# Performance work log

Hardware: AMD Instinct MI355X
Metric: run time of the kernel (lower is better)

## Reference

```python
import jax, jax.numpy as jnp
import numpy as np

EPS = 1e-5

def layer_norm(x, gamma, beta):
    mu = jnp.mean(x, axis=-1, keepdims=True)
    var = jnp.mean(jnp.square(x - mu), axis=-1, keepdims=True)
    return (x - mu) * jax.lax.rsqrt(var + EPS) * gamma + beta

def setup_inputs() -> dict:
    key = jax.random.key(0)
    ks = jax.random.split(key, 16)
    B, Cq, Hq, Wq = 8, 256, 32, 32
    Cc, Hc, Wc = 512, 64, 64
    def lin(k, fan_in, fan_out):
        lim = 1.0 / np.sqrt(fan_in)
        k1, k2 = jax.random.split(k)
        W = jax.random.uniform(k1, (fan_in, fan_out), jnp.float32, -lim, lim)
        b = jax.random.uniform(k2, (fan_out,), jnp.float32, -lim, lim)
        return W, b
    Wq_, bq = lin(ks[0], Cq, Cq)
    Wk_, bk = lin(ks[1], Cc, Cq)
    Wv_, bv = lin(ks[2], Cc, Cq)
    Wo_, bo = lin(ks[3], Cq, Cq)
    return {
        "query": jax.random.normal(ks[4], (B, Cq, Hq, Wq), jnp.float32),
        "context": jax.random.normal(ks[5], (B, Cc, Hc, Wc), jnp.float32),
        "Wq": Wq_, "bq": bq, "Wk": Wk_, "bk": bk, "Wv": Wv_, "bv": bv,
        "Wo": Wo_, "bo": bo,
        "gq": jnp.ones((Cq,), jnp.float32), "betq": jnp.zeros((Cq,), jnp.float32),
        "gc": jnp.ones((Cc,), jnp.float32), "betc": jnp.zeros((Cc,), jnp.float32),
    }

def reference(query, context, Wq, bq, Wk, bk, Wv, bv, Wo, bo, gq, betq, gc, betc):
    B, Cq, Hq, Wq_sp = query.shape
    _, Cc, Hc, Wc = context.shape
    num_heads = 8
    head_dim = Cq // num_heads
    scale = jnp.sqrt(jnp.float32(head_dim))
    N = Hq * Wq_sp
    # adaptive_avg_pool2d with divisible sizes == average pooling over equal bins
    ctx = context.reshape(B, Cc, Hq, Hc // Hq, Wq_sp, Wc // Wq_sp).mean(axis=(3, 5))
    q_flat = query.reshape(B, Cq, N).transpose(0, 2, 1)          # (B,N,Cq)
    c_flat = ctx.reshape(B, Cc, N).transpose(0, 2, 1)            # (B,N,Cc)
    qn = layer_norm(q_flat, gq, betq)
    cn = layer_norm(c_flat, gc, betc)
    q = (qn @ Wq + bq).reshape(B, N, num_heads, head_dim).transpose(0, 2, 1, 3)
    k = (cn @ Wk + bk).reshape(B, N, num_heads, head_dim).transpose(0, 2, 1, 3)
    v = (cn @ Wv + bv).reshape(B, N, num_heads, head_dim).transpose(0, 2, 1, 3)
    attn = jnp.einsum('bhnd,bhmd->bhnm', q, k) / scale
    attn = jax.nn.softmax(attn, axis=-1)
    out = jnp.einsum('bhnm,bhmd->bhnd', attn, v)
    out = out.transpose(0, 2, 1, 3).reshape(B, N, Cq)
    out = out @ Wo + bo
    out = q_flat + out                                           # residual
    return out.transpose(0, 2, 1).reshape(B, Cq, Hq, Wq_sp)
```

## Files before the change

### kernel.cpp

```cpp
#include <hip/hip_runtime.h>
#include <hip/hip_bf16.h>
#include <cstddef>

#define B_  8
#define CQ  256
#define CC  512
#define N_  1024
#define HQ  32
#define WQ  32
#define NH  8
#define HD  32

typedef __bf16 bf16x8 __attribute__((ext_vector_type(8)));
typedef float f32x4 __attribute__((ext_vector_type(4)));
typedef float f32x16 __attribute__((ext_vector_type(16)));
typedef unsigned int uint4v __attribute__((ext_vector_type(4)));
typedef unsigned short ushort8 __attribute__((ext_vector_type(8)));
typedef unsigned short ushort4v __attribute__((ext_vector_type(4)));

__device__ __forceinline__ unsigned short f2bf(float x) {
    return __builtin_bit_cast(unsigned short, __float2bfloat16(x));
}
__device__ __forceinline__ float bf2f(unsigned short x) {
    return __bfloat162float(__builtin_bit_cast(__hip_bfloat16, x));
}
__device__ __forceinline__ bf16x8 ldb8(const unsigned short* p) {
    return __builtin_bit_cast(bf16x8, *(const ushort8*)p);
}

__global__ __launch_bounds__(256) void prep_k(
    const float* __restrict__ query, const float* __restrict__ context,
    const float* __restrict__ Wq, const float* __restrict__ Wk,
    const float* __restrict__ Wv, const float* __restrict__ Wo,
    const float* __restrict__ gq, const float* __restrict__ betq,
    const float* __restrict__ gc, const float* __restrict__ betc,
    __hip_bfloat16* __restrict__ Wqt, __hip_bfloat16* __restrict__ Wkt,
    __hip_bfloat16* __restrict__ Wvt, __hip_bfloat16* __restrict__ Wot,
    __hip_bfloat16* __restrict__ qn, __hip_bfloat16* __restrict__ cn) {
    __shared__ float T[32][33];
    __shared__ float SsA[32][16];
    __shared__ float S2A[32][16];
    __shared__ float SsB[16][64];
    __shared__ float S2B[16][64];
    __shared__ float Mu[64], Rs[64];

    const int bid = blockIdx.x;
    const int tid = threadIdx.x;

    if (bid < 512) {
        const int x = bid & 15, y = (bid >> 4) & 7, z = bid >> 7;
        const float* W; __hip_bfloat16* Wt; int K;
        switch (z) {
            case 0: W = Wq; Wt = Wqt; K = CQ; break;
            case 1: W = Wk; Wt = Wkt; K = CC; break;
            case 2: W = Wv; Wt = Wvt; K = CC; break;
            default: W = Wo; Wt = Wot; K = CQ; break;
        }
        const int k0 = x * 32;
        if (k0 >= K) return;
        const int c0 = y * 32;
        const int tx = tid & 31, ty = tid >> 5;
        #pragma unroll
        for (int i = 0; i < 4; ++i) {
            const int r = ty + 8 * i;
            T[r][tx] = W[(size_t)(k0 + r) * CQ + c0 + tx];
        }
        __syncthreads();
        #pragma unroll
        for (int i = 0; i < 4; ++i) {
            const int r = ty + 8 * i;
            Wt[(size_t)(c0 + r) * K + k0 + tx] = __float2bfloat16(T[tx][r]);
        }
    } else if (bid < 1024) {
        const int u    = bid - 512;
        const int wqc2 = u & 1, hq = (u >> 1) & 31, b = u >> 6;
        const int pp   = tid & 7;
        const int cg   = tid >> 3;
        const int ch0  = cg * 16;

        const float* Cb = context + ((size_t)b * CC + ch0) * 4096
                        + (size_t)(2 * hq) * 64 + (32 * wqc2 + 4 * pp);
        float pv0[16], pv1[16];
        float ss0 = 0.f, ss1 = 0.f, s20 = 0.f, s21 = 0.f;
        #pragma unroll
        for (int i = 0; i < 16; ++i) {
            const float4 r0 = *(const float4*)(Cb + (size_t)i * 4096);
            const float4 r1 = *(const float4*)(Cb + (size_t)i * 4096 + 64);
            const float v0 = (r0.x + r0.y + r1.x + r1.y) * 0.25f;
            const float v1 = (r0.z + r0.w + r1.z + r1.w) * 0.25f;
            pv0[i] = v0; pv1[i] = v1;
            ss0 += v0; s20 += v0 * v0;
            ss1 += v1; s21 += v1 * v1;
        }
        SsA[cg][2 * pp]     = ss0; S2A[cg][2 * pp]     = s20;
        SsA[cg][2 * pp + 1] = ss1; S2A[cg][2 * pp + 1] = s21;
        __syncthreads();
        if (tid < 16) {
            float ts = 0.f, t2 = 0.f;
            #pragma unroll
            for (int i = 0; i < 32; ++i) { ts += SsA[i][tid]; t2 += S2A[i][tid]; }
            const float mu  = ts * (1.f / CC);
            const float var = t2 * (1.f / CC) - mu * mu;
            Mu[tid] = mu; Rs[tid] = rsqrtf(var + 1e-5f);
        }
        __syncthreads();
        const float mu0 = Mu[2 * pp],     rs0 = Rs[2 * pp];
        const float mu1 = Mu[2 * pp + 1], rs1 = Rs[2 * pp + 1];
        const int pos0 = hq * 32 + wqc2 * 16 + 2 * pp;
        unsigned short* dst = (unsigned short*)cn
            + ((size_t)b * N_ + pos0) * CC + ch0;
        ushort8 a0, a1, b0, b1;
        #pragma unroll
        for (int i = 0; i < 8; ++i) {
            a0[i] = f2bf((pv0[i] - mu0) * rs0 * gc[ch0 + i] + betc[ch0 + i]);
            b0[i] = f2bf((pv1[i] - mu1) * rs1 * gc[ch0 + i] + betc[ch0 + i]);
        }
        #pragma unroll
        for (int i = 0; i < 8; ++i) {
            a1[i] = f2bf((pv0[8 + i] - mu0) * rs0 * gc[ch0 + 8 + i] + betc[ch0 + 8 + i]);
            b1[i] = f2bf((pv1[8 + i] - mu1) * rs1 * gc[ch0 + 8 + i] + betc[ch0 + 8 + i]);
        }
        *(ushort8*)(dst)          = a0;
        *(ushort8*)(dst + 8)      = a1;
        *(ushort8*)(dst + CC)     = b0;
        *(ushort8*)(dst + CC + 8) = b1;
    } else {
        const int u  = bid - 1024;
        const int nt = u & 15, b = u >> 4;
        const int nq = tid & 15;
        const int cg = tid >> 4;
        const int ch0 = cg * 16;
        const int nb  = nt * 64 + 4 * nq;

        const float* Qb = query + ((size_t)b * CQ + ch0) * N_ + nb;
        float qv[64];
        float ps[4] = {0.f, 0.f, 0.f, 0.f};
        float p2[4] = {0.f, 0.f, 0.f, 0.f};
        #pragma unroll
        for (int i = 0; i < 16; ++i) {
            const float4 v = *(const float4*)(Qb + (size_t)i * N_);
            qv[4 * i + 0] = v.x; qv[4 * i + 1] = v.y;
            qv[4 * i + 2] = v.z; qv[4 * i + 3] = v.w;
            ps[0] += v.x; p2[0] += v.x * v.x;
            ps[1] += v.y; p2[1] += v.y * v.y;
            ps[2] += v.z; p2[2] += v.z * v.z;
            ps[3] += v.w; p2[3] += v.w * v.w;
        }
        #pragma unroll
        for (int j = 0; j < 4; ++j) {
            SsB[cg][4 * nq + j] = ps[j];
            S2B[cg][4 * nq + j] = p2[j];
        }
        __syncthreads();
        if (tid < 64) {
            float ts = 0.f, t2 = 0.f;
            #pragma unroll
            for (int i = 0; i < 16; ++i) { ts += SsB[i][tid]; t2 += S2B[i][tid]; }
            const float mu  = ts * (1.f / CQ);
            const float var = t2 * (1.f / CQ) - mu * mu;
            Mu[tid] = mu; Rs[tid] = rsqrtf(var + 1e-5f);
        }
        __syncthreads();
        #pragma unroll
        for (int j = 0; j < 4; ++j) {
            const float mu = Mu[4 * nq + j], rs = Rs[4 * nq + j];
            ushort8 o0, o1;
            #pragma unroll
            for (int i = 0; i < 8; ++i)
                o0[i] = f2bf((qv[4 * i + j] - mu) * rs * gq[ch0 + i] + betq[ch0 + i]);
            #pragma unroll
            for (int i = 0; i < 8; ++i)
                o1[i] = f2bf((qv[4 * (8 + i) + j] - mu) * rs * gq[ch0 + 8 + i] + betq[ch0 + 8 + i]);
            unsigned short* dst = (unsigned short*)qn
                + ((size_t)b * N_ + nb + j) * CQ + ch0;
            *(ushort8*)(dst)     = o0;
            *(ushort8*)(dst + 8) = o1;
        }
    }
}

__global__ __launch_bounds__(256) void proj_all_k(
    const __hip_bfloat16* __restrict__ qn, const __hip_bfloat16* __restrict__ cn,
    const __hip_bfloat16* __restrict__ Wqt, const __hip_bfloat16* __restrict__ Wkt,
    const __hip_bfloat16* __restrict__ Wvt,
    const float* __restrict__ bq, const float* __restrict__ bk,
    const float* __restrict__ bv,
    __hip_bfloat16* __restrict__ Qb, __hip_bfloat16* __restrict__ Kb,
    __hip_bfloat16* __restrict__ Vt, float qsc) {
    __shared__ unsigned short As[64][40];
    __shared__ unsigned short B1[64][40];
    __shared__ unsigned short B2[64][40];

    const int zz = blockIdx.z;
    const int n0 = blockIdx.x * 64;
    const int c0 = blockIdx.y * 64;
    const int tid = threadIdx.x;
    const int wid = tid >> 6, lane = tid & 63;
    const int lg = lane >> 4, ln = lane & 15;
    const int wn0 = (wid & 1) * 32, wc0 = (wid >> 1) * 32;
    const int sr = tid >> 2;
    const int sk = (tid & 3) * 8;

    if (zz >= 8) {
        const int b = zz - 8;
        const unsigned short* Ab = (const unsigned short*)qn + ((size_t)b * N_ + n0) * CQ;
        const unsigned short* Wb = (const unsigned short*)Wqt + (size_t)c0 * CQ;
        f32x4 acc[2][2] = {};
        ushort8 ra = *(const ushort8*)(Ab + (size_t)sr * CQ + sk);
        ushort8 rw = *(const ushort8*)(Wb + (size_t)sr * CQ + sk);
        for (int t = 0; t < 8; ++t) {
            *(ushort8*)&As[sr][sk] = ra;
            *(ushort8*)&B1[sr][sk] = rw;
            __syncthreads();
            if (t < 7) {
                ra = *(const ushort8*)(Ab + (size_t)sr * CQ + (t + 1) * 32 + sk);
                rw = *(const ushort8*)(Wb + (size_t)sr * CQ + (t + 1) * 32 + sk);
            }
            bf16x8 a[2], w[2];
            #pragma unroll
            for (int i = 0; i < 2; ++i) a[i] = ldb8(&As[wn0 + 16 * i + ln][8 * lg]);
            #pragma unroll
            for (int j = 0; j < 2; ++j) w[j] = ldb8(&B1[wc0 + 16 * j + ln][8 * lg]);
            #pragma unroll
            for (int i = 0; i < 2; ++i)
                #pragma unroll
                for (int j = 0; j < 2; ++j)
                    acc[i][j] = __builtin_amdgcn_mfma_f32_16x16x32_bf16(a[i], w[j], acc[i][j], 0, 0, 0);
            __syncthreads();
        }
        #pragma unroll
        for (int j = 0; j < 2; ++j) {
            const int co = c0 + wc0 + 16 * j + ln;
            const int h = co >> 5, d = co & 31;
            const float bb = bq[co];
            #pragma unroll
            for (int i = 0; i < 2; ++i)
                #pragma unroll
                for (int r = 0; r < 4; ++r) {
                    const int n = n0 + wn0 + 16 * i + 4 * lg + r;
                    Qb[(((size_t)b * NH + h) * N_ + n) * HD + d] =
                        __float2bfloat16((acc[i][j][r] + bb) * qsc);
                }
        }
    } else {
        const int b = zz;
        const unsigned short* Ab  = (const unsigned short*)cn + ((size_t)b * N_ + n0) * CC;
        const unsigned short* Wkb = (const unsigned short*)Wkt + (size_t)c0 * CC;
        const unsigned short* Wvb = (const unsigned short*)Wvt + (size_t)c0 * CC;
        f32x4 accK[2][2] = {};
        f32x4 accV[2][2] = {};
        ushort8 ra = *(const ushort8*)(Ab  + (size_t)sr * CC + sk);
        ushort8 rk = *(const ushort8*)(Wkb + (size_t)sr * CC + sk);
        ushort8 rv = *(const ushort8*)(Wvb + (size_t)sr * CC + sk);
        for (int t = 0; t < 16; ++t) {
            *(ushort8*)&As[sr][sk] = ra;
            *(ushort8*)&B1[sr][sk] = rk;
            *(ushort8*)&B2[sr][sk] = rv;
            __syncthreads();
            if (t < 15) {
                ra = *(const ushort8*)(Ab  + (size_t)sr * CC + (t + 1) * 32 + sk);
                rk = *(const ushort8*)(Wkb + (size_t)sr * CC + (t + 1) * 32 + sk);
                rv = *(const ushort8*)(Wvb + (size_t)sr * CC + (t + 1) * 32 + sk);
            }
            bf16x8 a[2], wk[2], wv[2];
            #pragma unroll
            for (int i = 0; i < 2; ++i) {
                a[i]  = ldb8(&As[wn0 + 16 * i + ln][8 * lg]);
                wk[i] = ldb8(&B1[wc0 + 16 * i + ln][8 * lg]);
                wv[i] = ldb8(&B2[wc0 + 16 * i + ln][8 * lg]);
            }
            #pragma unroll
            for (int i = 0; i < 2; ++i)
                #pragma unroll
                for (int j = 0; j < 2; ++j) {
                    accK[i][j] = __builtin_amdgcn_mfma_f32_16x16x32_bf16(a[i], wk[j], accK[i][j], 0, 0, 0);
                    accV[i][j] = __builtin_amdgcn_mfma_f32_16x16x32_bf16(a[i], wv[j], accV[i][j], 0, 0, 0);
                }
            __syncthreads();
        }
        #pragma unroll
        for (int j = 0; j < 2; ++j) {
            const int co = c0 + wc0 + 16 * j + ln;
            const int h = co >> 5, d = co & 31;
            const float bbk = bk[co], bbv = bv[co];
            #pragma unroll
            for (int i = 0; i < 2; ++i) {
                const int nb = n0 + wn0 + 16 * i + 4 * lg;
                #pragma unroll
                for (int r = 0; r < 4; ++r)
                    Kb[(((size_t)b * NH + h) * N_ + nb + r) * HD + d] =
                        __float2bfloat16(accK[i][j][r] + bbk);
                ushort4v o;
                #pragma unroll
                for (int r = 0; r < 4; ++r) o[r] = f2bf(accV[i][j][r] + bbv);
                const int g  = (nb >> 2) & 3;
                const int gp = ((g & 1) << 1) | (g >> 1);
                const int nbp = (nb & ~15) | (gp << 2);
                *(ushort4v*)((unsigned short*)Vt + (((size_t)b * NH + h) * HD + d) * N_ + nbp) = o;
            }
        }
    }
}

__global__ __launch_bounds__(256) void attn32_k(
    const __hip_bfloat16* __restrict__ Q,
    const __hip_bfloat16* __restrict__ K,
    const __hip_bfloat16* __restrict__ Vt,
    __hip_bfloat16* __restrict__ O) {
    __shared__ float accS[2][64][20];
    __shared__ float lwS[2][64];

    const int lin = blockIdx.x + 16 * blockIdx.y;
    const int eff = (lin & 7) * 128 + (lin >> 3);
    const int qt  = eff & 15;
    const int bh  = eff >> 4;
    const int b   = bh >> 3;
    const int h   = bh & 7;
    const int wid  = threadIdx.x >> 6;
    const int lane = threadIdx.x & 63;
    const int l31  = lane & 31;
    const int hh   = lane >> 5;
    const int qsub = wid >> 1;
    const int kvh  = wid & 1;
    const int q0   = qt * 64 + qsub * 32;

    const unsigned short* Qp = (const unsigned short*)Q + ((size_t)bh * N_ + q0) * HD;
    const unsigned short* Kbb = (const unsigned short*)K + (size_t)bh * N_ * HD;
    const unsigned short* Vb = (const unsigned short*)Vt + ((size_t)bh * HD + l31) * N_;

    bf16x8 qB[2];
    #pragma unroll
    for (int m = 0; m < 2; ++m)
        qB[m] = ldb8(Qp + (size_t)l31 * HD + 16 * m + 8 * hh);

    const f32x16 Z = {0.f,0.f,0.f,0.f,0.f,0.f,0.f,0.f,
                      0.f,0.f,0.f,0.f,0.f,0.f,0.f,0.f};
    f32x16 acc = Z;
    float ls0 = 0.f, ls1 = 0.f, ls2 = 0.f, ls3 = 0.f;

    const int kvbase = kvh * 512;
    const unsigned short* kp = Kbb + (size_t)(kvbase + l31) * HD + 8 * hh;
    const unsigned short* vp = Vb + kvbase + 8 * hh;

    bf16x8 kaA[2][4];
    #pragma unroll
    for (int j = 0; j < 4; ++j)
        kaA[0][j] = ldb8(kp + (j >> 1) * 1024 + (j & 1) * 16);

    #pragma unroll
    for (int st = 0; st < 8; ++st) {
        const int cur = st & 1;
        bf16x8 va[4];
        #pragma unroll
        for (int j = 0; j < 4; ++j)
            va[j] = ldb8(vp + st * 64 + 16 * j);
        if (st < 7) {
            const unsigned short* kp2 = kp + (size_t)(st + 1) * 2048;
            #pragma unroll
            for (int j = 0; j < 4; ++j)
                kaA[cur ^ 1][j] = ldb8(kp2 + (j >> 1) * 1024 + (j & 1) * 16);
        }

        f32x16 s0, s1;
        s0 = __builtin_amdgcn_mfma_f32_32x32x16_bf16(kaA[cur][0], qB[0], Z, 0, 0, 0);
        s0 = __builtin_amdgcn_mfma_f32_32x32x16_bf16(kaA[cur][1], qB[1], s0, 0, 0, 0);
        s1 = __builtin_amdgcn_mfma_f32_32x32x16_bf16(kaA[cur][2], qB[0], Z, 0, 0, 0);
        s1 = __builtin_amdgcn_mfma_f32_32x32x16_bf16(kaA[cur][3], qB[1], s1, 0, 0, 0);

        unsigned int pk[2][4][2];
        #pragma unroll
        for (int T = 0; T < 2; ++T) {
            float p[16];
            #pragma unroll
            for (int r = 0; r < 16; ++r)
                p[r] = __builtin_amdgcn_exp2f(T == 0 ? s0[r] : s1[r]);
            #pragma unroll
            for (int r = 0; r < 16; r += 4) {
                ls0 += p[r]; ls1 += p[r + 1]; ls2 += p[r + 2]; ls3 += p[r + 3];
            }
            #pragma unroll
            for (int c = 0; c < 4; ++c) {
                asm("v_cvt_pk_bf16_f32 %0, %1, %2"
                    : "=v"(pk[T][c][0]) : "v"(p[4 * c]), "v"(p[4 * c + 1]));
                asm("v_cvt_pk_bf16_f32 %0, %1, %2"
                    : "=v"(pk[T][c][1]) : "v"(p[4 * c + 2]), "v"(p[4 * c + 3]));
            }
        }

        #pragma unroll
        for (int w = 0; w < 4; ++w) {
            const int T = w >> 1, cp = w & 1;
            uint4v fu = {pk[T][2 * cp][0], pk[T][2 * cp][1],
                         pk[T][2 * cp + 1][0], pk[T][2 * cp + 1][1]};
            const bf16x8 pa = __builtin_bit_cast(bf16x8, fu);
            acc = __builtin_amdgcn_mfma_f32_32x32x16_bf16(pa, va[w], acc, 0, 0, 0);
        }
    }

    const float lsum = (ls0 + ls1) + (ls2 + ls3);
    const float lw = lsum + __shfl_xor(lsum, 32);

    if (kvh == 1) {
        #pragma unroll
        for (int r4 = 0; r4 < 4; ++r4) {
            float4 v = {acc[4 * r4], acc[4 * r4 + 1], acc[4 * r4 + 2], acc[4 * r4 + 3]};
            *(float4*)&accS[qsub][lane][4 * r4] = v;
        }
        lwS[qsub][lane] = lw;
    }
    __syncthreads();
    if (kvh == 0) {
        const float linv = 1.0f / (lw + lwS[qsub][lane]);
        #pragma unroll
        for (int r = 0; r < 16; ++r) {
            const int ql = (r & 3) + 8 * (r >> 2) + 4 * hh;
            const float vv = (acc[r] + accS[qsub][lane][r]) * __shfl(linv, ql);
            O[((size_t)b * N_ + q0 + ql) * CQ + h * HD + l31] = __float2bfloat16(vv);
        }
    }
}

__global__ __launch_bounds__(256) void out_proj_k(const __hip_bfloat16* __restrict__ Ob,
                              const __hip_bfloat16* __restrict__ Wot,
                              const float* __restrict__ bo,
                              const float* __restrict__ query,
                              float* __restrict__ out) {
    __shared__ unsigned short As[64][40];
    __shared__ unsigned short Bs[64][40];
    const int b  = blockIdx.z;
    const int n0 = blockIdx.x * 64;
    const int c0 = blockIdx.y * 64;
    const int tid = threadIdx.x;
    const int wid = tid >> 6, lane = tid & 63;
    const int lg = lane >> 4, ln = lane & 15;
    const int wn0 = (wid & 1) * 32, wc0 = (wid >> 1) * 32;

    const unsigned short* Ab = (const unsigned short*)Ob + ((size_t)b * N_ + n0) * CQ;
    const unsigned short* Wb = (const unsigned short*)Wot + (size_t)c0 * CQ;
    const int sr = tid >> 2;
    const int sk = (tid & 3) * 8;

    f32x4 acc[2][2] = {};
    ushort8 ra = *(const ushort8*)(Ab + (size_t)sr * CQ + sk);
    ushort8 rw = *(const ushort8*)(Wb + (size_t)sr * CQ + sk);

    for (int t = 0; t < 8; ++t) {
        *(ushort8*)&As[sr][sk] = ra;
        *(ushort8*)&Bs[sr][sk] = rw;
        __syncthreads();
        if (t < 7) {
            ra = *(const ushort8*)(Ab + (size_t)sr * CQ + (t + 1) * 32 + sk);
            rw = *(const ushort8*)(Wb + (size_t)sr * CQ + (t + 1) * 32 + sk);
        }
        bf16x8 a[2], w[2];
        #pragma unroll
        for (int i = 0; i < 2; ++i)
            a[i] = ldb8(&As[wn0 + 16 * i + ln][8 * lg]);
        #pragma unroll
        for (int j = 0; j < 2; ++j)
            w[j] = ldb8(&Bs[wc0 + 16 * j + ln][8 * lg]);
        #pragma unroll
        for (int i = 0; i < 2; ++i)
            #pragma unroll
            for (int j = 0; j < 2; ++j)
                acc[i][j] = __builtin_amdgcn_mfma_f32_16x16x32_bf16(a[i], w[j], acc[i][j], 0, 0, 0);
        __syncthreads();
    }

    #pragma unroll
    for (int j = 0; j < 2; ++j) {
        const int co = c0 + wc0 + 16 * j + ln;
        const float bb = bo[co];
        #pragma unroll
        for (int i = 0; i < 2; ++i) {
            const int nb = n0 + wn0 + 16 * i + 4 * lg;
            const float4 res = *(const float4*)&query[((size_t)b * CQ + co) * N_ + nb];
            float4 o;
            o.x = acc[i][j][0] + bb + res.x;
            o.y = acc[i][j][1] + bb + res.y;
            o.z = acc[i][j][2] + bb + res.z;
            o.w = acc[i][j][3] + bb + res.w;
            *(float4*)&out[((size_t)b * CQ + co) * N_ + nb] = o;
        }
    }
}

extern "C" void kernel_launch(void* const* d_in, const int* in_sizes, int n_in,
                              void* d_out, int out_size, void* d_ws, size_t ws_size,
                              hipStream_t stream) {
    const float* query   = (const float*)d_in[0];
    const float* context = (const float*)d_in[1];
    const float* Wq = (const float*)d_in[2];
    const float* bq = (const float*)d_in[3];
    const float* Wk = (const float*)d_in[4];
    const float* bk = (const float*)d_in[5];
    const float* Wv = (const float*)d_in[6];
    const float* bv = (const float*)d_in[7];
    const float* Wo = (const float*)d_in[8];
    const float* bo = (const float*)d_in[9];
    const float* gq   = (const float*)d_in[10];
    const float* betq = (const float*)d_in[11];
    const float* gc   = (const float*)d_in[12];
    const float* betc = (const float*)d_in[13];
    float* out = (float*)d_out;

    char* w = (char*)d_ws;
    __hip_bfloat16* qn  = (__hip_bfloat16*)w;  w += (size_t)B_ * N_ * CQ * 2;
    __hip_bfloat16* cn  = (__hip_bfloat16*)w;  w += (size_t)B_ * N_ * CC * 2;
    __hip_bfloat16* Qb  = (__hip_bfloat16*)w;  w += (size_t)B_ * NH * N_ * HD * 2;
    __hip_bfloat16* Kb  = (__hip_bfloat16*)w;  w += (size_t)B_ * NH * N_ * HD * 2;
    __hip_bfloat16* Vt  = (__hip_bfloat16*)w;  w += (size_t)B_ * NH * HD * N_ * 2;
    __hip_bfloat16* Ob  = (__hip_bfloat16*)w;  w += (size_t)B_ * N_ * CQ * 2;
    __hip_bfloat16* Wqt = (__hip_bfloat16*)w;  w += (size_t)CQ * CQ * 2;
    __hip_bfloat16* Wkt = (__hip_bfloat16*)w;  w += (size_t)CQ * CC * 2;
    __hip_bfloat16* Wvt = (__hip_bfloat16*)w;  w += (size_t)CQ * CC * 2;
    __hip_bfloat16* Wot = (__hip_bfloat16*)w;  w += (size_t)CQ * CQ * 2;

    prep_k<<<dim3(1152), 256, 0, stream>>>(query, context, Wq, Wk, Wv, Wo,
                                           gq, betq, gc, betc,
                                           Wqt, Wkt, Wvt, Wot, qn, cn);

    const float qsc = 0.17677669529663687f * 1.4426950408889634f;
    proj_all_k<<<dim3(16, 4, 16), 256, 0, stream>>>(qn, cn, Wqt, Wkt, Wvt,
                                                    bq, bk, bv, Qb, Kb, Vt, qsc);

    attn32_k<<<dim3(16, 64), 256, 0, stream>>>(Qb, Kb, Vt, Ob);

    out_proj_k<<<dim3(16, 4, 8), 256, 0, stream>>>(Ob, Wot, bo, query, out);
}
```

Before: 66.68 us.

## Fuse layernorm and pooling into Q/K/V projection kernel, drop normalized intermediates

Splits weight transposition into its own kernel and fuses context pooling, both layernorms and the Q/K/V projection GEMMs into one kernel. Each 16-row tile is normalized into swizzled shared memory and multiplied against bf16 weights read directly from global memory with MFMA, so the qn/cn buffers are never written to or read back from HBM. In exchange, each block now uses small 16-row tiles that re-read the full weight matrices from global or L2 without shared-memory staging, which could make the projection limited by weight bandwidth.

Result: slower. 95.26 us (+42.9%).

```diff
diff --git a/kernel.cpp b/kernel.cpp
--- a/kernel.cpp
+++ b/kernel.cpp
@@ -21,65 +21,71 @@
 __device__ __forceinline__ unsigned short f2bf(float x) {
     return __builtin_bit_cast(unsigned short, __float2bfloat16(x));
 }
-__device__ __forceinline__ float bf2f(unsigned short x) {
-    return __bfloat162float(__builtin_bit_cast(__hip_bfloat16, x));
-}
 __device__ __forceinline__ bf16x8 ldb8(const unsigned short* p) {
     return __builtin_bit_cast(bf16x8, *(const ushort8*)p);
 }
 
-__global__ __launch_bounds__(256) void prep_k(
-    const float* __restrict__ query, const float* __restrict__ context,
+__global__ __launch_bounds__(256) void wt_conv_all_k(
     const float* __restrict__ Wq, const float* __restrict__ Wk,
     const float* __restrict__ Wv, const float* __restrict__ Wo,
+    __hip_bfloat16* __restrict__ Wqt, __hip_bfloat16* __restrict__ Wkt,
+    __hip_bfloat16* __restrict__ Wvt, __hip_bfloat16* __restrict__ Wot) {
+    __shared__ float T[32][33];
+    const float* W; __hip_bfloat16* Wt; int K;
+    switch (blockIdx.z) {
+        case 0: W = Wq; Wt = Wqt; K = CQ; break;
+        case 1: W = Wk; Wt = Wkt; K = CC; break;
+        case 2: W = Wv; Wt = Wvt; K = CC; break;
+        default: W = Wo; Wt = Wot; K = CQ; break;
+    }
+    const int k0 = blockIdx.x * 32;
+    if (k0 >= K) return;
+    const int c0 = blockIdx.y * 32;
+    const int tx = threadIdx.x & 31;
+    const int ty = threadIdx.x >> 5;
+    #pragma unroll
+    for (int i = 0; i < 4; ++i) {
+        const int r = ty + 8 * i;
+        T[r][tx] = W[(size_t)(k0 + r) * CQ + c0 + tx];
+    }
+    __syncthreads();
+    #pragma unroll
+    for (int i = 0; i < 4; ++i) {
+        const int r = ty + 8 * i;
+        Wt[(size_t)(c0 + r) * K + k0 + tx] = __float2bfloat16(T[tx][r]);
+    }
+}
+
+__global__ __launch_bounds__(256) void fused_proj_k(
+    const float* __restrict__ query, const float* __restrict__ context,
+    const __hip_bfloat16* __restrict__ Wqt, const __hip_bfloat16* __restrict__ Wkt,
+    const __hip_bfloat16* __restrict__ Wvt,
+    const float* __restrict__ bq, const float* __restrict__ bk,
+    const float* __restrict__ bv,
     const float* __restrict__ gq, const float* __restrict__ betq,
     const float* __restrict__ gc, const float* __restrict__ betc,
-    __hip_bfloat16* __restrict__ Wqt, __hip_bfloat16* __restrict__ Wkt,
-    __hip_bfloat16* __restrict__ Wvt, __hip_bfloat16* __restrict__ Wot,
-    __hip_bfloat16* __restrict__ qn, __hip_bfloat16* __restrict__ cn) {
-    __shared__ float T[32][33];
-    __shared__ float SsA[32][16];
-    __shared__ float S2A[32][16];
-    __shared__ float SsB[16][64];
-    __shared__ float S2B[16][64];
-    __shared__ float Mu[64], Rs[64];
+    __hip_bfloat16* __restrict__ Qb, __hip_bfloat16* __restrict__ Kb,
+    __hip_bfloat16* __restrict__ Vt, float qsc) {
+    __shared__ __align__(16) unsigned short Asm[16 * 512];
+    __shared__ float Ss[64][16];
+    __shared__ float S2s[64][16];
+    __shared__ float Mu[16], Rs[16];
 
     const int bid = blockIdx.x;
     const int tid = threadIdx.x;
+    const int wid = tid >> 6, lane = tid & 63;
+    const int lg = lane >> 4, ln = lane & 15;
 
     if (bid < 512) {
-        const int x = bid & 15, y = (bid >> 4) & 7, z = bid >> 7;
-        const float* W; __hip_bfloat16* Wt; int K;
-        switch (z) {
-            case 0: W = Wq; Wt = Wqt; K = CQ; break;
-            case 1: W = Wk; Wt = Wkt; K = CC; break;
-            case 2: W = Wv; Wt = Wvt; K = CC; break;
-            default: W = Wo; Wt = Wot; K = CQ; break;
-        }
-        const int k0 = x * 32;
-        if (k0 >= K) return;
-        const int c0 = y * 32;
-        const int tx = tid & 31, ty = tid >> 5;
-        #pragma unroll
-        for (int i = 0; i < 4; ++i) {
-            const int r = ty + 8 * i;
-            T[r][tx] = W[(size_t)(k0 + r) * CQ + c0 + tx];
-        }
-        __syncthreads();
-        #pragma unroll
-        for (int i = 0; i < 4; ++i) {
-            const int r = ty + 8 * i;
-            Wt[(size_t)(c0 + r) * K + k0 + tx] = __float2bfloat16(T[tx][r]);
-        }
-    } else if (bid < 1024) {
-        const int u    = bid - 512;
-        const int wqc2 = u & 1, hq = (u >> 1) & 31, b = u >> 6;
-        const int pp   = tid & 7;
-        const int cg   = tid >> 3;
-        const int ch0  = cg * 16;
-
+        const int n0t = bid & 63, b = bid >> 6;
+        const int hq = n0t >> 1, wqh = (n0t & 1) * 16;
+        const int n0 = n0t * 16;
+
+        const int pp = tid & 7;
+        const int cg = tid >> 3;
+        const int ch0 = cg * 16;
         const float* Cb = context + ((size_t)b * CC + ch0) * 4096
-                        + (size_t)(2 * hq) * 64 + (32 * wqc2 + 4 * pp);
+                        + (size_t)(2 * hq) * 64 + (2 * wqh + 4 * pp);
         float pv0[16], pv1[16];
         float ss0 = 0.f, ss1 = 0.f, s20 = 0.f, s21 = 0.f;
         #pragma unroll
@@ -92,70 +98,106 @@
             ss0 += v0; s20 += v0 * v0;
             ss1 += v1; s21 += v1 * v1;
         }
-        SsA[cg][2 * pp]     = ss0; S2A[cg][2 * pp]     = s20;
-        SsA[cg][2 * pp + 1] = ss1; S2A[cg][2 * pp + 1] = s21;
+        Ss[cg][2 * pp]      = ss0; S2s[cg][2 * pp]      = s20;
+        Ss[cg][2 * pp + 1]  = ss1; S2s[cg][2 * pp + 1]  = s21;
         __syncthreads();
         if (tid < 16) {
             float ts = 0.f, t2 = 0.f;
             #pragma unroll
-            for (int i = 0; i < 32; ++i) { ts += SsA[i][tid]; t2 += S2A[i][tid]; }
+            for (int i = 0; i < 32; ++i) { ts += Ss[i][tid]; t2 += S2s[i][tid]; }
             const float mu  = ts * (1.f / CC);
             const float var = t2 * (1.f / CC) - mu * mu;
             Mu[tid] = mu; Rs[tid] = rsqrtf(var + 1e-5f);
         }
         __syncthreads();
-        const float mu0 = Mu[2 * pp],     rs0 = Rs[2 * pp];
-        const float mu1 = Mu[2 * pp + 1], rs1 = Rs[2 * pp + 1];
-        const int pos0 = hq * 32 + wqc2 * 16 + 2 * pp;
-        unsigned short* dst = (unsigned short*)cn
-            + ((size_t)b * N_ + pos0) * CC + ch0;
-        ushort8 a0, a1, b0, b1;
-        #pragma unroll
-        for (int i = 0; i < 8; ++i) {
-            a0[i] = f2bf((pv0[i] - mu0) * rs0 * gc[ch0 + i] + betc[ch0 + i]);
-            b0[i] = f2bf((pv1[i] - mu1) * rs1 * gc[ch0 + i] + betc[ch0 + i]);
-        }
-        #pragma unroll
-        for (int i = 0; i < 8; ++i) {
-            a1[i] = f2bf((pv0[8 + i] - mu0) * rs0 * gc[ch0 + 8 + i] + betc[ch0 + 8 + i]);
-            b1[i] = f2bf((pv1[8 + i] - mu1) * rs1 * gc[ch0 + 8 + i] + betc[ch0 + 8 + i]);
-        }
-        *(ushort8*)(dst)          = a0;
-        *(ushort8*)(dst + 8)      = a1;
-        *(ushort8*)(dst + CC)     = b0;
-        *(ushort8*)(dst + CC + 8) = b1;
+
+        {
+            const int lp0 = 2 * pp, lp1 = 2 * pp + 1;
+            const float mu0 = Mu[lp0], rs0 = Rs[lp0];
+            const float mu1 = Mu[lp1], rs1 = Rs[lp1];
+            #pragma unroll
+            for (int cc = 0; cc < 2; ++cc) {
+                ushort8 o0, o1;
+                #pragma unroll
+                for (int e = 0; e < 8; ++e) {
+                    const int ch = ch0 + 8 * cc + e;
+                    o0[e] = f2bf((pv0[8 * cc + e] - mu0) * rs0 * gc[ch] + betc[ch]);
+                    o1[e] = f2bf((pv1[8 * cc + e] - mu1) * rs1 * gc[ch] + betc[ch]);
+                }
+                const int ch8 = 2 * cg + cc;
+                *(ushort8*)&Asm[lp0 * 512 + ((ch8 ^ (lp0 & 7)) * 8)] = o0;
+                *(ushort8*)&Asm[lp1 * 512 + ((ch8 ^ (lp1 & 7)) * 8)] = o1;
+            }
+        }
+        __syncthreads();
+
+        const int isV = wid >> 1;
+        const int wc0 = (wid & 1) * 128;
+        const unsigned short* WtB = (const unsigned short*)(isV ? Wvt : Wkt);
+        const float* bias = isV ? bv : bk;
+
+        f32x4 acc[8] = {};
+        #pragma unroll 4
+        for (int t = 0; t < 16; ++t) {
+            const int k0 = 32 * t;
+            const int chunk = (4 * t + lg) ^ (ln & 7);
+            const bf16x8 af = ldb8(&Asm[ln * 512 + chunk * 8]);
+            #pragma unroll
+            for (int j = 0; j < 8; ++j) {
+                const bf16x8 wf = ldb8(WtB + (size_t)(wc0 + 16 * j + ln) * CC + k0 + 8 * lg);
+                acc[j] = __builtin_amdgcn_mfma_f32_16x16x32_bf16(af, wf, acc[j], 0, 0, 0);
+            }
+        }
+
+        #pragma unroll
+        for (int j = 0; j < 8; ++j) {
+            const int co = wc0 + 16 * j + ln;
+            const int h = co >> 5, d = co & 31;
+            const float bb = bias[co];
+            if (!isV) {
+                #pragma unroll
+                for (int r = 0; r < 4; ++r)
+                    Kb[(((size_t)b * NH + h) * N_ + n0 + 4 * lg + r) * HD + d] =
+                        __float2bfloat16(acc[j][r] + bb);
+            } else {
+                const int gp = ((lg & 1) << 1) | (lg >> 1);
+                ushort4v o;
+                #pragma unroll
+                for (int r = 0; r < 4; ++r) o[r] = f2bf(acc[j][r] + bb);
+                *(ushort4v*)((unsigned short*)Vt
+                    + (((size_t)b * NH + h) * HD + d) * N_ + n0 + 4 * gp) = o;
+            }
+        }
     } else {
-        const int u  = bid - 1024;
-        const int nt = u & 15, b = u >> 4;
-        const int nq = tid & 15;
-        const int cg = tid >> 4;
-        const int ch0 = cg * 16;
-        const int nb  = nt * 64 + 4 * nq;
-
-        const float* Qb = query + ((size_t)b * CQ + ch0) * N_ + nb;
-        float qv[64];
-        float ps[4] = {0.f, 0.f, 0.f, 0.f};
-        float p2[4] = {0.f, 0.f, 0.f, 0.f};
-        #pragma unroll
-        for (int i = 0; i < 16; ++i) {
-            const float4 v = *(const float4*)(Qb + (size_t)i * N_);
-            qv[4 * i + 0] = v.x; qv[4 * i + 1] = v.y;
-            qv[4 * i + 2] = v.z; qv[4 * i + 3] = v.w;
-            ps[0] += v.x; p2[0] += v.x * v.x;
-            ps[1] += v.y; p2[1] += v.y * v.y;
-            ps[2] += v.z; p2[2] += v.z * v.z;
-            ps[3] += v.w; p2[3] += v.w * v.w;
+        const int u = bid - 512;
+        const int n0t = u & 63, b = u >> 6;
+        const int n0 = n0t * 16;
+
+        const int n4 = tid & 3;
+        const int cg = tid >> 2;
+        const float* Qrow = query + ((size_t)b * CQ + 4 * cg) * N_ + n0 + 4 * n4;
+        float qv[4][4];
+        float sj[4] = {0.f, 0.f, 0.f, 0.f};
+        float s2j[4] = {0.f, 0.f, 0.f, 0.f};
+        #pragma unroll
+        for (int i = 0; i < 4; ++i) {
+            const float4 v = *(const float4*)(Qrow + (size_t)i * N_);
+            qv[i][0] = v.x; qv[i][1] = v.y; qv[i][2] = v.z; qv[i][3] = v.w;
+            sj[0] += v.x; s2j[0] += v.x * v.x;
+            sj[1] += v.y; s2j[1] += v.y * v.y;
+            sj[2] += v.z; s2j[2] += v.z * v.z;
+            sj[3] += v.w; s2j[3] += v.w * v.w;
         }
         #pragma unroll
         for (int j = 0; j < 4; ++j) {
-            SsB[cg][4 * nq + j] = ps[j];
-            S2B[cg][4 * nq + j] = p2[j];
-        }
-        __syncthreads();
-        if (tid < 64) {
+            Ss[cg][4 * n4 + j] = sj[j];
+            S2s[cg][4 * n4 + j] = s2j[j];
+        }
+        __syncthreads();
+        if (tid < 16) {
             float ts = 0.f, t2 = 0.f;
             #pragma unroll
-            for (int i = 0; i < 16; ++i) { ts += SsB[i][tid]; t2 += S2B[i][tid]; }
+            for (int i = 0; i < 64; ++i) { ts += Ss[i][tid]; t2 += S2s[i][tid]; }
             const float mu  = ts * (1.f / CQ);
             const float var = t2 * (1.f / CQ) - mu * mu;
             Mu[tid] = mu; Rs[tid] = rsqrtf(var + 1e-5f);
@@ -163,141 +205,41 @@
         __syncthreads();
         #pragma unroll
         for (int j = 0; j < 4; ++j) {
-            const float mu = Mu[4 * nq + j], rs = Rs[4 * nq + j];
-            ushort8 o0, o1;
-            #pragma unroll
-            for (int i = 0; i < 8; ++i)
-                o0[i] = f2bf((qv[4 * i + j] - mu) * rs * gq[ch0 + i] + betq[ch0 + i]);
-            #pragma unroll
-            for (int i = 0; i < 8; ++i)
-                o1[i] = f2bf((qv[4 * (8 + i) + j] - mu) * rs * gq[ch0 + 8 + i] + betq[ch0 + 8 + i]);
-            unsigned short* dst = (unsigned short*)qn
-                + ((size_t)b * N_ + nb + j) * CQ + ch0;
-            *(ushort8*)(dst)     = o0;
-            *(ushort8*)(dst + 8) = o1;
-        }
-    }
-}
-
-__global__ __launch_bounds__(256) void proj_all_k(
-    const __hip_bfloat16* __restrict__ qn, const __hip_bfloat16* __restrict__ cn,
-    const __hip_bfloat16* __restrict__ Wqt, const __hip_bfloat16* __restrict__ Wkt,
-    const __hip_bfloat16* __restrict__ Wvt,
-    const float* __restrict__ bq, const float* __restrict__ bk,
-    const float* __restrict__ bv,
-    __hip_bfloat16* __restrict__ Qb, __hip_bfloat16* __restrict__ Kb,
-    __hip_bfloat16* __restrict__ Vt, float qsc) {
-    __shared__ unsigned short As[64][40];
-    __shared__ unsigned short B1[64][40];
-    __shared__ unsigned short B2[64][40];
-
-    const int zz = blockIdx.z;
-    const int n0 = blockIdx.x * 64;
-    const int c0 = blockIdx.y * 64;
-    const int tid = threadIdx.x;
-    const int wid = tid >> 6, lane = tid & 63;
-    const int lg = lane >> 4, ln = lane & 15;
-    const int wn0 = (wid & 1) * 32, wc0 = (wid >> 1) * 32;
-    const int sr = tid >> 2;
-    const int sk = (tid & 3) * 8;
-
-    if (zz >= 8) {
-        const int b = zz - 8;
-        const unsigned short* Ab = (const unsigned short*)qn + ((size_t)b * N_ + n0) * CQ;
-        const unsigned short* Wb = (const unsigned short*)Wqt + (size_t)c0 * CQ;
-        f32x4 acc[2][2] = {};
-        ushort8 ra = *(const ushort8*)(Ab + (size_t)sr * CQ + sk);
-        ushort8 rw = *(const ushort8*)(Wb + (size_t)sr * CQ + sk);
+            const int row = 4 * n4 + j;
+            const float mu = Mu[row], rs = Rs[row];
+            ushort4v o;
+            #pragma unroll
+            for (int i = 0; i < 4; ++i) {
+                const int ch = 4 * cg + i;
+                o[i] = f2bf((qv[i][j] - mu) * rs * gq[ch] + betq[ch]);
+            }
+            *(ushort4v*)&Asm[row * 256 + (((cg >> 1) ^ (row & 7)) * 8) + (cg & 1) * 4] = o;
+        }
+        __syncthreads();
+
+        const int wc0 = wid * 64;
+        const unsigned short* WtB = (const unsigned short*)Wqt;
+        f32x4 acc[4] = {};
+        #pragma unroll 4
         for (int t = 0; t < 8; ++t) {
-            *(ushort8*)&As[sr][sk] = ra;
-            *(ushort8*)&B1[sr][sk] = rw;
-            __syncthreads();
-            if (t < 7) {
-                ra = *(const ushort8*)(Ab + (size_t)sr * CQ + (t + 1) * 32 + sk);
-                rw = *(const ushort8*)(Wb + (size_t)sr * CQ + (t + 1) * 32 + sk);
-            }
-            bf16x8 a[2], w[2];
-            #pragma unroll
-            for (int i = 0; i < 2; ++i) a[i] = ldb8(&As[wn0 + 16 * i + ln][8 * lg]);
-            #pragma unroll
-            for (int j = 0; j < 2; ++j) w[j] = ldb8(&B1[wc0 + 16 * j + ln][8 * lg]);
-            #pragma unroll
-            for (int i = 0; i < 2; ++i)
-                #pragma unroll
-                for (int j = 0; j < 2; ++j)
-                    acc[i][j] = __builtin_amdgcn_mfma_f32_16x16x32_bf16(a[i], w[j], acc[i][j], 0, 0, 0);
-            __syncthreads();
-        }
-        #pragma unroll
-        for (int j = 0; j < 2; ++j) {
-            const int co = c0 + wc0 + 16 * j + ln;
+            const int k0 = 32 * t;
+            const int chunk = (4 * t + lg) ^ (ln & 7);
+            const bf16x8 af = ldb8(&Asm[ln * 256 + chunk * 8]);
+            #pragma unroll
+            for (int j = 0; j < 4; ++j) {
+                const bf16x8 wf = ldb8(WtB + (size_t)(wc0 + 16 * j + ln) * CQ + k0 + 8 * lg);
+                acc[j] = __builtin_amdgcn_mfma_f32_16x16x32_bf16(af, wf, acc[j], 0, 0, 0);
+            }
+        }
+        #pragma unroll
+        for (int j = 0; j < 4; ++j) {
+            const int co = wc0 + 16 * j + ln;
             const int h = co >> 5, d = co & 31;
             const float bb = bq[co];
             #pragma unroll
-            for (int i = 0; i < 2; ++i)
-                #pragma unroll
-                for (int r = 0; r < 4; ++r) {
-                    const int n = n0 + wn0 + 16 * i + 4 * lg + r;
-                    Qb[(((size_t)b * NH + h) * N_ + n) * HD + d] =
-                        __float2bfloat16((acc[i][j][r] + bb) * qsc);
-                }
-        }
-    } else {
-        const int b = zz;
-        const unsigned short* Ab  = (const unsigned short*)cn + ((size_t)b * N_ + n0) * CC;
-        const unsigned short* Wkb = (const unsigned short*)Wkt + (size_t)c0 * CC;
-        const unsigned short* Wvb = (const unsigned short*)Wvt + (size_t)c0 * CC;
-        f32x4 accK[2][2] = {};
-        f32x4 accV[2][2] = {};
-        ushort8 ra = *(const ushort8*)(Ab  + (size_t)sr * CC + sk);
-        ushort8 rk = *(const ushort8*)(Wkb + (size_t)sr * CC + sk);
-        ushort8 rv = *(const ushort8*)(Wvb + (size_t)sr * CC + sk);
-        for (int t = 0; t < 16; ++t) {
-            *(ushort8*)&As[sr][sk] = ra;
-            *(ushort8*)&B1[sr][sk] = rk;
-            *(ushort8*)&B2[sr][sk] = rv;
-            __syncthreads();
-            if (t < 15) {
-                ra = *(const ushort8*)(Ab  + (size_t)sr * CC + (t + 1) * 32 + sk);
-                rk = *(const ushort8*)(Wkb + (size_t)sr * CC + (t + 1) * 32 + sk);
-                rv = *(const ushort8*)(Wvb + (size_t)sr * CC + (t + 1) * 32 + sk);
-            }
-            bf16x8 a[2], wk[2], wv[2];
-            #pragma unroll
-            for (int i = 0; i < 2; ++i) {
-                a[i]  = ldb8(&As[wn0 + 16 * i + ln][8 * lg]);
-                wk[i] = ldb8(&B1[wc0 + 16 * i + ln][8 * lg]);
-                wv[i] = ldb8(&B2[wc0 + 16 * i + ln][8 * lg]);
-            }
-            #pragma unroll
-            for (int i = 0; i < 2; ++i)
-                #pragma unroll
-                for (int j = 0; j < 2; ++j) {
-                    accK[i][j] = __builtin_amdgcn_mfma_f32_16x16x32_bf16(a[i], wk[j], accK[i][j], 0, 0, 0);
-                    accV[i][j] = __builtin_amdgcn_mfma_f32_16x16x32_bf16(a[i], wv[j], accV[i][j], 0, 0, 0);
-                }
-            __syncthreads();
-        }
-        #pragma unroll
-        for (int j = 0; j < 2; ++j) {
-            const int co = c0 + wc0 + 16 * j + ln;
-            const int h = co >> 5, d = co & 31;
-            const float bbk = bk[co], bbv = bv[co];
-            #pragma unroll
-            for (int i = 0; i < 2; ++i) {
-                const int nb = n0 + wn0 + 16 * i + 4 * lg;
-                #pragma unroll
-                for (int r = 0; r < 4; ++r)
-                    Kb[(((size_t)b * NH + h) * N_ + nb + r) * HD + d] =
-                        __float2bfloat16(accK[i][j][r] + bbk);
-                ushort4v o;
-                #pragma unroll
-                for (int r = 0; r < 4; ++r) o[r] = f2bf(accV[i][j][r] + bbv);
-                const int g  = (nb >> 2) & 3;
-                const int gp = ((g & 1) << 1) | (g >> 1);
-                const int nbp = (nb & ~15) | (gp << 2);
-                *(ushort4v*)((unsigned short*)Vt + (((size_t)b * NH + h) * HD + d) * N_ + nbp) = o;
-            }
+            for (int r = 0; r < 4; ++r)
+                Qb[(((size_t)b * NH + h) * N_ + n0 + 4 * lg + r) * HD + d] =
+                    __float2bfloat16((acc[j][r] + bb) * qsc);
         }
     }
 }
@@ -505,8 +447,6 @@
     float* out = (float*)d_out;
 
     char* w = (char*)d_ws;
-    __hip_bfloat16* qn  = (__hip_bfloat16*)w;  w += (size_t)B_ * N_ * CQ * 2;
-    __hip_bfloat16* cn  = (__hip_bfloat16*)w;  w += (size_t)B_ * N_ * CC * 2;
     __hip_bfloat16* Qb  = (__hip_bfloat16*)w;  w += (size_t)B_ * NH * N_ * HD * 2;
     __hip_bfloat16* Kb  = (__hip_bfloat16*)w;  w += (size_t)B_ * NH * N_ * HD * 2;
     __hip_bfloat16* Vt  = (__hip_bfloat16*)w;  w += (size_t)B_ * NH * HD * N_ * 2;
@@ -516,13 +456,15 @@
     __hip_bfloat16* Wvt = (__hip_bfloat16*)w;  w += (size_t)CQ * CC * 2;
     __hip_bfloat16* Wot = (__hip_bfloat16*)w;  w += (size_t)CQ * CQ * 2;
 
-    prep_k<<<dim3(1152), 256, 0, stream>>>(query, context, Wq, Wk, Wv, Wo,
-                                           gq, betq, gc, betc,
-                                           Wqt, Wkt, Wvt, Wot, qn, cn);
+    wt_conv_all_k<<<dim3(16, 8, 4), 256, 0, stream>>>(Wq, Wk, Wv, Wo,
+                                                      Wqt, Wkt, Wvt, Wot);
 
     const float qsc = 0.17677669529663687f * 1.4426950408889634f;
-    proj_all_k<<<dim3(16, 4, 16), 256, 0, stream>>>(qn, cn, Wqt, Wkt, Wvt,
-                                                    bq, bk, bv, Qb, Kb, Vt, qsc);
+    fused_proj_k<<<dim3(1024), 256, 0, stream>>>(query, context,
+                                                 Wqt, Wkt, Wvt,
+                                                 bq, bk, bv,
+                                                 gq, betq, gc, betc,
+                                                 Qb, Kb, Vt, qsc);
 
     attn32_k<<<dim3(16, 64), 256, 0, stream>>>(Qb, Kb, Vt, Ob);
 
```

## Split attention KV across four waves per query tile and halve pooling block work

Applied to the files above, without the earlier changes.

The attention kernel now gives each block a single 32-query tile and splits the 1024 keys across all four waves, 256 keys each. Partial outputs and row sums are reduced through shared memory, and the grid doubles to 2048 blocks. The context pooling plus layernorm stage now covers 8 positions per block instead of 16, using 1024 blocks, which raises parallelism and lowers per-thread register use. The cost is more cross-wave reduction traffic and sync per query, plus redundant Q loads across blocks.

Result: slower. 76.73 us (+15.1%).

```diff
diff --git a/kernel.cpp b/kernel.cpp
--- a/kernel.cpp
+++ b/kernel.cpp
@@ -20,9 +20,6 @@
 
 __device__ __forceinline__ unsigned short f2bf(float x) {
     return __builtin_bit_cast(unsigned short, __float2bfloat16(x));
-}
-__device__ __forceinline__ float bf2f(unsigned short x) {
-    return __bfloat162float(__builtin_bit_cast(__hip_bfloat16, x));
 }
 __device__ __forceinline__ bf16x8 ldb8(const unsigned short* p) {
     return __builtin_bit_cast(bf16x8, *(const ushort8*)p);
@@ -38,8 +35,8 @@
     __hip_bfloat16* __restrict__ Wvt, __hip_bfloat16* __restrict__ Wot,
     __hip_bfloat16* __restrict__ qn, __hip_bfloat16* __restrict__ cn) {
     __shared__ float T[32][33];
-    __shared__ float SsA[32][16];
-    __shared__ float S2A[32][16];
+    __shared__ float SsA[64][16];
+    __shared__ float S2A[64][16];
     __shared__ float SsB[16][64];
     __shared__ float S2B[16][64];
     __shared__ float Mu[64], Rs[64];
@@ -71,19 +68,19 @@
             const int r = ty + 8 * i;
             Wt[(size_t)(c0 + r) * K + k0 + tx] = __float2bfloat16(T[tx][r]);
         }
-    } else if (bid < 1024) {
-        const int u    = bid - 512;
-        const int wqc2 = u & 1, hq = (u >> 1) & 31, b = u >> 6;
-        const int pp   = tid & 7;
-        const int cg   = tid >> 3;
-        const int ch0  = cg * 16;
+    } else if (bid < 1536) {
+        const int u   = bid - 512;
+        const int wq8 = u & 3, hq = (u >> 2) & 31, b = u >> 7;
+        const int pp  = tid & 3;
+        const int cg  = tid >> 2;
+        const int ch0 = cg * 8;
 
         const float* Cb = context + ((size_t)b * CC + ch0) * 4096
-                        + (size_t)(2 * hq) * 64 + (32 * wqc2 + 4 * pp);
-        float pv0[16], pv1[16];
+                        + (size_t)(2 * hq) * 64 + (16 * wq8 + 4 * pp);
+        float pv0[8], pv1[8];
         float ss0 = 0.f, ss1 = 0.f, s20 = 0.f, s21 = 0.f;
         #pragma unroll
-        for (int i = 0; i < 16; ++i) {
+        for (int i = 0; i < 8; ++i) {
             const float4 r0 = *(const float4*)(Cb + (size_t)i * 4096);
             const float4 r1 = *(const float4*)(Cb + (size_t)i * 4096 + 64);
             const float v0 = (r0.x + r0.y + r1.x + r1.y) * 0.25f;
@@ -95,10 +92,10 @@
         SsA[cg][2 * pp]     = ss0; S2A[cg][2 * pp]     = s20;
         SsA[cg][2 * pp + 1] = ss1; S2A[cg][2 * pp + 1] = s21;
         __syncthreads();
-        if (tid < 16) {
+        if (tid < 8) {
             float ts = 0.f, t2 = 0.f;
             #pragma unroll
-            for (int i = 0; i < 32; ++i) { ts += SsA[i][tid]; t2 += S2A[i][tid]; }
+            for (int i = 0; i < 64; ++i) { ts += SsA[i][tid]; t2 += S2A[i][tid]; }
             const float mu  = ts * (1.f / CC);
             const float var = t2 * (1.f / CC) - mu * mu;
             Mu[tid] = mu; Rs[tid] = rsqrtf(var + 1e-5f);
@@ -106,26 +103,19 @@
         __syncthreads();
         const float mu0 = Mu[2 * pp],     rs0 = Rs[2 * pp];
         const float mu1 = Mu[2 * pp + 1], rs1 = Rs[2 * pp + 1];
-        const int pos0 = hq * 32 + wqc2 * 16 + 2 * pp;
+        const int pos = hq * 32 + wq8 * 8 + 2 * pp;
         unsigned short* dst = (unsigned short*)cn
-            + ((size_t)b * N_ + pos0) * CC + ch0;
-        ushort8 a0, a1, b0, b1;
-        #pragma unroll
-        for (int i = 0; i < 8; ++i) {
-            a0[i] = f2bf((pv0[i] - mu0) * rs0 * gc[ch0 + i] + betc[ch0 + i]);
-            b0[i] = f2bf((pv1[i] - mu1) * rs1 * gc[ch0 + i] + betc[ch0 + i]);
-        }
-        #pragma unroll
-        for (int i = 0; i < 8; ++i) {
-            a1[i] = f2bf((pv0[8 + i] - mu0) * rs0 * gc[ch0 + 8 + i] + betc[ch0 + 8 + i]);
-            b1[i] = f2bf((pv1[8 + i] - mu1) * rs1 * gc[ch0 + 8 + i] + betc[ch0 + 8 + i]);
-        }
-        *(ushort8*)(dst)          = a0;
-        *(ushort8*)(dst + 8)      = a1;
-        *(ushort8*)(dst + CC)     = b0;
-        *(ushort8*)(dst + CC + 8) = b1;
+            + ((size_t)b * N_ + pos) * CC + ch0;
+        ushort8 o0, o1;
+        #pragma unroll
+        for (int e = 0; e < 8; ++e) {
+            o0[e] = f2bf((pv0[e] - mu0) * rs0 * gc[ch0 + e] + betc[ch0 + e]);
+            o1[e] = f2bf((pv1[e] - mu1) * rs1 * gc[ch0 + e] + betc[ch0 + e]);
+        }
+        *(ushort8*)(dst)      = o0;
+        *(ushort8*)(dst + CC) = o1;
     } else {
-        const int u  = bid - 1024;
+        const int u  = bid - 1536;
         const int nt = u & 15, b = u >> 4;
         const int nq = tid & 15;
         const int cg = tid >> 4;
@@ -307,22 +297,20 @@
     const __hip_bfloat16* __restrict__ K,
     const __hip_bfloat16* __restrict__ Vt,
     __hip_bfloat16* __restrict__ O) {
-    __shared__ float accS[2][64][20];
-    __shared__ float lwS[2][64];
-
-    const int lin = blockIdx.x + 16 * blockIdx.y;
-    const int eff = (lin & 7) * 128 + (lin >> 3);
-    const int qt  = eff & 15;
-    const int bh  = eff >> 4;
+    __shared__ float accS[3][64][20];
+    __shared__ float lwS[3][64];
+
+    const int lin = blockIdx.x + 32 * blockIdx.y;
+    const int eff = (lin & 7) * 256 + (lin >> 3);
+    const int qt  = eff & 31;
+    const int bh  = eff >> 5;
     const int b   = bh >> 3;
     const int h   = bh & 7;
     const int wid  = threadIdx.x >> 6;
     const int lane = threadIdx.x & 63;
     const int l31  = lane & 31;
     const int hh   = lane >> 5;
-    const int qsub = wid >> 1;
-    const int kvh  = wid & 1;
-    const int q0   = qt * 64 + qsub * 32;
+    const int q0   = qt * 32;
 
     const unsigned short* Qp = (const unsigned short*)Q + ((size_t)bh * N_ + q0) * HD;
     const unsigned short* Kbb = (const unsigned short*)K + (size_t)bh * N_ * HD;
@@ -338,7 +326,7 @@
     f32x16 acc = Z;
     float ls0 = 0.f, ls1 = 0.f, ls2 = 0.f, ls3 = 0.f;
 
-    const int kvbase = kvh * 512;
+    const int kvbase = wid * 256;
     const unsigned short* kp = Kbb + (size_t)(kvbase + l31) * HD + 8 * hh;
     const unsigned short* vp = Vb + kvbase + 8 * hh;
 
@@ -348,13 +336,13 @@
         kaA[0][j] = ldb8(kp + (j >> 1) * 1024 + (j & 1) * 16);
 
     #pragma unroll
-    for (int st = 0; st < 8; ++st) {
+    for (int st = 0; st < 4; ++st) {
         const int cur = st & 1;
         bf16x8 va[4];
         #pragma unroll
         for (int j = 0; j < 4; ++j)
             va[j] = ldb8(vp + st * 64 + 16 * j);
-        if (st < 7) {
+        if (st < 3) {
             const unsigned short* kp2 = kp + (size_t)(st + 1) * 2048;
             #pragma unroll
             for (int j = 0; j < 4; ++j)
@@ -400,21 +388,23 @@
     const float lsum = (ls0 + ls1) + (ls2 + ls3);
     const float lw = lsum + __shfl_xor(lsum, 32);
 
-    if (kvh == 1) {
+    if (wid > 0) {
         #pragma unroll
         for (int r4 = 0; r4 < 4; ++r4) {
             float4 v = {acc[4 * r4], acc[4 * r4 + 1], acc[4 * r4 + 2], acc[4 * r4 + 3]};
-            *(float4*)&accS[qsub][lane][4 * r4] = v;
-        }
-        lwS[qsub][lane] = lw;
+            *(float4*)&accS[wid - 1][lane][4 * r4] = v;
+        }
+        lwS[wid - 1][lane] = lw;
     }
     __syncthreads();
-    if (kvh == 0) {
-        const float linv = 1.0f / (lw + lwS[qsub][lane]);
+    if (wid == 0) {
+        const float ltot = lw + lwS[0][lane] + lwS[1][lane] + lwS[2][lane];
+        const float linv = 1.0f / ltot;
         #pragma unroll
         for (int r = 0; r < 16; ++r) {
             const int ql = (r & 3) + 8 * (r >> 2) + 4 * hh;
-            const float vv = (acc[r] + accS[qsub][lane][r]) * __shfl(linv, ql);
+            const float vv = (acc[r] + accS[0][lane][r] + accS[1][lane][r]
+                              + accS[2][lane][r]) * __shfl(linv, ql);
             O[((size_t)b * N_ + q0 + ql) * CQ + h * HD + l31] = __float2bfloat16(vv);
         }
     }
@@ -516,7 +506,7 @@
     __hip_bfloat16* Wvt = (__hip_bfloat16*)w;  w += (size_t)CQ * CC * 2;
     __hip_bfloat16* Wot = (__hip_bfloat16*)w;  w += (size_t)CQ * CQ * 2;
 
-    prep_k<<<dim3(1152), 256, 0, stream>>>(query, context, Wq, Wk, Wv, Wo,
+    prep_k<<<dim3(1664), 256, 0, stream>>>(query, context, Wq, Wk, Wv, Wo,
                                            gq, betq, gc, betc,
                                            Wqt, Wkt, Wvt, Wot, qn, cn);
 
@@ -524,7 +514,7 @@
     proj_all_k<<<dim3(16, 4, 16), 256, 0, stream>>>(qn, cn, Wqt, Wkt, Wvt,
                                                     bq, bk, bv, Qb, Kb, Vt, qsc);
 
-    attn32_k<<<dim3(16, 64), 256, 0, stream>>>(Qb, Kb, Vt, Ob);
+    attn32_k<<<dim3(32, 64), 256, 0, stream>>>(Qb, Kb, Vt, Ob);
 
     out_proj_k<<<dim3(16, 4, 8), 256, 0, stream>>>(Ob, Wot, bo, query, out);
 }
```
